# Kernel tuning notes

Hardware: AMD Instinct MI355X
Metric: run time of the kernel (lower is better)

## Reference

```python
import jax, jax.numpy as jnp
import numpy as np

B, S, D = 4, 2048, 1024
H = 16
KD = 1024  # key_dim (total)
VD = 1024  # value_dim (total)


def setup_inputs() -> dict:
    key = jax.random.key(0)
    ks = jax.random.split(key, 8)
    queries = jax.random.normal(ks[0], (B, S, D), dtype=jnp.float32)
    keys_ = jax.random.normal(ks[1], (B, S, D), dtype=jnp.float32)
    values = jax.random.normal(ks[2], (B, S, D), dtype=jnp.float32)
    # causal float mask (1 = keep, 0 = masked), broadcasts over [B, H, S, S]
    mask = jnp.tril(jnp.ones((S, S), dtype=jnp.float32))[None, None]
    # Linear weights stored as [in, out] so forward is x @ W
    Wq = jax.random.normal(ks[3], (D, KD), dtype=jnp.float32) / np.sqrt(D)
    Wk = jax.random.normal(ks[4], (D, KD), dtype=jnp.float32) / np.sqrt(D)
    Wv = jax.random.normal(ks[5], (D, VD), dtype=jnp.float32) / np.sqrt(D)
    Wo = jax.random.normal(ks[6], (H * VD // H * H // H * 1 if False else VD, D), dtype=jnp.float32) / np.sqrt(VD)
    bo = jnp.zeros((D,), dtype=jnp.float32)
    return {"queries": queries, "keys": keys_, "values": values, "mask": mask,
            "Wq": Wq, "Wk": Wk, "Wv": Wv, "Wo": Wo, "bo": bo}


def reference(queries, keys, values, mask, Wq, Wk, Wv, Wo, bo):
    b, s, _ = queries.shape
    # project then split heads: [B, S, H, hd] -> [B, H, S, hd]
    q = (queries @ Wq).reshape(b, s, H, -1).transpose(0, 2, 1, 3)
    k = (keys @ Wk).reshape(b, s, H, -1).transpose(0, 2, 1, 3)
    v = (values @ Wv).reshape(b, s, H, -1).transpose(0, 2, 1, 3)
    dk = k.shape[-1]  # per-head key dim (scale uses post-split dk, as in source)
    logits = jnp.einsum('bhqd,bhkd->bhqk', q, k) / jnp.sqrt(jnp.float32(dk))
    logits = logits + (1.0 - mask) * (-1e9)
    attn = jax.nn.softmax(logits, axis=-1)  # dropout p=0 in eval -> identity
    o = jnp.einsum('bhqk,bhkd->bhqd', attn, v)
    o = o.transpose(0, 2, 1, 3).reshape(b, s, H * (VD // H))
    return o @ Wo + bo
```

## Files before the change

kernel.cpp:

```cpp
#include <hip/hip_runtime.h>
#include <hip/hip_bf16.h>

typedef __attribute__((ext_vector_type(8))) short s8v;
typedef __attribute__((ext_vector_type(4))) short s4v;
typedef __attribute__((ext_vector_type(4))) float f4v;

#define S_LEN 2048
#define NH 16
#define HD 64
#define DMODEL 1024
#define KVB 64
#define LOG2E 1.44269504088896f
#define FIXMAX 32.0f

__device__ __forceinline__ unsigned short f2bf(float f) {
  union { float f; unsigned int u; } v; v.f = f;
  return (unsigned short)((v.u + 0x7FFFu + ((v.u >> 16) & 1u)) >> 16);
}

__device__ __forceinline__ f4v mfma16(s8v a, s8v b, f4v c) {
  return __builtin_amdgcn_mfma_f32_16x16x32_bf16(a, b, c, 0, 0, 0);
}

__device__ __forceinline__ void gl_lds16(const unsigned short* g, unsigned short* l) {
  __builtin_amdgcn_global_load_lds(
      (const __attribute__((address_space(1))) void*)g,
      (__attribute__((address_space(3))) void*)l, 16, 0, 0);
}

__global__ __launch_bounds__(256)
void cast3(const float* __restrict__ a, const float* __restrict__ b,
           const float* __restrict__ c, unsigned short* __restrict__ oa,
           unsigned short* __restrict__ ob, unsigned short* __restrict__ oc,
           int n8) {
  const float* src = (blockIdx.y == 0) ? a : (blockIdx.y == 1) ? b : c;
  unsigned short* dst = (blockIdx.y == 0) ? oa : (blockIdx.y == 1) ? ob : oc;
  for (int i = blockIdx.x * 256 + threadIdx.x; i < n8; i += gridDim.x * 256) {
    f4v v0 = *(const f4v*)(src + (size_t)i * 8);
    f4v v1 = *(const f4v*)(src + (size_t)i * 8 + 4);
    unsigned short cv[8];
#pragma unroll
    for (int j = 0; j < 4; j++) { cv[j] = f2bf(v0[j]); cv[4 + j] = f2bf(v1[j]); }
    *(s8v*)(dst + (size_t)i * 8) = *(const s8v*)cv;
  }
}

__global__ __launch_bounds__(256)
void transpose_cast4(const float* __restrict__ w0, const float* __restrict__ w1,
                     const float* __restrict__ w2, const float* __restrict__ w3,
                     unsigned short* __restrict__ o0, unsigned short* __restrict__ o1,
                     unsigned short* __restrict__ o2, unsigned short* __restrict__ o3) {
  __shared__ float tile[32][33];
  const int z = blockIdx.z;
  const float* W = (z == 0) ? w0 : (z == 1) ? w1 : (z == 2) ? w2 : w3;
  unsigned short* Wt = (z == 0) ? o0 : (z == 1) ? o1 : (z == 2) ? o2 : o3;
  int x = threadIdx.x, y = threadIdx.y;
  int n0 = blockIdx.x * 32, k0 = blockIdx.y * 32;
#pragma unroll
  for (int i = 0; i < 32; i += 8)
    tile[y + i][x] = W[(size_t)(k0 + y + i) * DMODEL + n0 + x];
  __syncthreads();
#pragma unroll
  for (int i = 0; i < 32; i += 8)
    Wt[(size_t)(n0 + y + i) * DMODEL + k0 + x] = f2bf(tile[x][y + i]);
}

__global__ __launch_bounds__(256, 2)
void qkv_gemm(const unsigned short* __restrict__ Qc, const unsigned short* __restrict__ Kc,
              const unsigned short* __restrict__ Vc, const unsigned short* __restrict__ WqT,
              const unsigned short* __restrict__ WkT, const unsigned short* __restrict__ WvT,
              unsigned short* __restrict__ Qb, unsigned short* __restrict__ Kb,
              unsigned short* __restrict__ Vtb) {
  __shared__ unsigned short As[128 * 32];
  __shared__ unsigned short Bs[128 * 32];
  const int z = blockIdx.z;
  const unsigned short* A = (z == 0) ? Qc : (z == 1) ? Kc : Vc;
  const unsigned short* Bt = (z == 0) ? WqT : (z == 1) ? WkT : WvT;
  unsigned short* C = (z == 0) ? Qb : (z == 1) ? Kb : Vtb;
  const float scale = (z == 0) ? 0.125f * LOG2E : 1.0f;

  const int t = threadIdx.x;
  const int l = t & 63;
  const int w = t >> 6, wr = w >> 1, wc = w & 1;
  const int m0 = blockIdx.x * 128, n0 = blockIdx.y * 128;
  const int lg = l >> 4, lm = l & 15;

  f4v acc[4][4];
#pragma unroll
  for (int i = 0; i < 4; i++)
#pragma unroll
    for (int j = 0; j < 4; j++) acc[i][j] = f4v{0.f, 0.f, 0.f, 0.f};

  const int srow = t >> 2;
  const int scol = (t & 3) * 8;
  const unsigned short* Arow = A + (size_t)(m0 + srow) * DMODEL + scol;
  const unsigned short* Brow = Bt + (size_t)(n0 + srow) * DMODEL + scol;
  unsigned short* AsW = &As[w * 512];
  unsigned short* BsW = &Bs[w * 512];

  for (int k0 = 0; k0 < DMODEL; k0 += 32) {
    gl_lds16(Arow + k0, AsW);
    gl_lds16(Arow + (size_t)64 * DMODEL + k0, AsW + 2048);
    gl_lds16(Brow + k0, BsW);
    gl_lds16(Brow + (size_t)64 * DMODEL + k0, BsW + 2048);
    __syncthreads();

    s8v af[4], bf[4];
#pragma unroll
    for (int mi = 0; mi < 4; mi++)
      af[mi] = *(const s8v*)&As[(wr * 64 + mi * 16 + lm) * 32 + lg * 8];
#pragma unroll
    for (int ni = 0; ni < 4; ni++)
      bf[ni] = *(const s8v*)&Bs[(wc * 64 + ni * 16 + lm) * 32 + lg * 8];
#pragma unroll
    for (int mi = 0; mi < 4; mi++)
#pragma unroll
      for (int ni = 0; ni < 4; ni++)
        acc[mi][ni] = mfma16(af[mi], bf[ni], acc[mi][ni]);
    __syncthreads();
  }

#pragma unroll
  for (int mi = 0; mi < 4; mi++)
#pragma unroll
    for (int ni = 0; ni < 4; ni++) {
      int col = n0 + wc * 64 + ni * 16 + lm;
#pragma unroll
      for (int rr = 0; rr < 4; rr++) {
        int row = m0 + wr * 64 + mi * 16 + lg * 4 + rr;
        unsigned short h = f2bf(acc[mi][ni][rr] * scale);
        int b = row >> 11, s = row & 2047, hh = col >> 6, d = col & 63;
        if (z < 2)
          C[(((size_t)(b * NH + hh)) * S_LEN + s) * HD + d] = h;
        else
          C[(((size_t)(b * NH + hh)) * HD + d) * S_LEN + s] = h;
      }
    }
}

__global__ __launch_bounds__(256, 2)
void out_gemm(const unsigned short* __restrict__ A, const unsigned short* __restrict__ Bt,
              float* __restrict__ Cp, const float* __restrict__ bias) {
  __shared__ unsigned short As[128 * 32];
  __shared__ unsigned short Bs[128 * 32];
  const int t = threadIdx.x;
  const int l = t & 63;
  const int w = t >> 6, wr = w >> 1, wc = w & 1;
  const int m0 = blockIdx.x * 128, n0 = blockIdx.y * 128;
  const int lg = l >> 4, lm = l & 15;

  f4v acc[4][4];
#pragma unroll
  for (int i = 0; i < 4; i++)
#pragma unroll
    for (int j = 0; j < 4; j++) acc[i][j] = f4v{0.f, 0.f, 0.f, 0.f};

  const int srow = t >> 2;
  const int scol = (t & 3) * 8;
  const unsigned short* Arow = A + (size_t)(m0 + srow) * DMODEL + scol;
  const unsigned short* Brow = Bt + (size_t)(n0 + srow) * DMODEL + scol;
  unsigned short* AsW = &As[w * 512];
  unsigned short* BsW = &Bs[w * 512];

  for (int k0 = 0; k0 < DMODEL; k0 += 32) {
    gl_lds16(Arow + k0, AsW);
    gl_lds16(Arow + (size_t)64 * DMODEL + k0, AsW + 2048);
    gl_lds16(Brow + k0, BsW);
    gl_lds16(Brow + (size_t)64 * DMODEL + k0, BsW + 2048);
    __syncthreads();

    s8v af[4], bf[4];
#pragma unroll
    for (int mi = 0; mi < 4; mi++)
      af[mi] = *(const s8v*)&As[(wr * 64 + mi * 16 + lm) * 32 + lg * 8];
#pragma unroll
    for (int ni = 0; ni < 4; ni++)
      bf[ni] = *(const s8v*)&Bs[(wc * 64 + ni * 16 + lm) * 32 + lg * 8];
#pragma unroll
    for (int mi = 0; mi < 4; mi++)
#pragma unroll
      for (int ni = 0; ni < 4; ni++)
        acc[mi][ni] = mfma16(af[mi], bf[ni], acc[mi][ni]);
    __syncthreads();
  }

#pragma unroll
  for (int mi = 0; mi < 4; mi++)
#pragma unroll
    for (int ni = 0; ni < 4; ni++) {
      int col = n0 + wc * 64 + ni * 16 + lm;
      float bv = bias[col];
#pragma unroll
      for (int rr = 0; rr < 4; rr++) {
        int row = m0 + wr * 64 + mi * 16 + lg * 4 + rr;
        Cp[(size_t)row * DMODEL + col] = acc[mi][ni][rr] + bv;
      }
    }
}

__global__ __launch_bounds__(256, 2)
void attn_k(const unsigned short* __restrict__ Q, const unsigned short* __restrict__ Km,
            const unsigned short* __restrict__ Vt, unsigned short* __restrict__ O) {
  __shared__ unsigned short Ks[2][KVB * HD];
  __shared__ unsigned short Vs[2][HD * KVB];
  __shared__ unsigned short pbuf[16][16 * KVB];
  const int t = threadIdx.x, l = t & 63, w = t >> 6;
  const int lg = l >> 4, lm = l & 15;

  const int c = blockIdx.x;
  const int bh = c & 63;
  const int pr4 = (c >> 6) & 3;
  const int pr = (c >> 8) ? 7 - pr4 : pr4;
  const int s0A = (15 - pr) * 128, s0B = pr * 128;

  const unsigned short* Qh = Q + (size_t)bh * S_LEN * HD;
  const unsigned short* Kh = Km + (size_t)bh * S_LEN * HD;
  const unsigned short* Vh = Vt + (size_t)bh * HD * S_LEN;

  const int xo0 = (lg ^ (lm & 7)) << 4;
  const int xo1 = ((4 + lg) ^ (lm & 7)) << 4;

  const int q00 = s0A + w * 32, q01 = q00 + 16;
  const int q02 = s0B + w * 32, q03 = q02 + 16;

  s8v qf0[2], qf1[2], qf2[2], qf3[2];
#define LOADQ(QF, Q0)                                                   \
  QF[0] = *(const s8v*)(Qh + (size_t)((Q0) + lm) * HD + lg * 8);        \
  QF[1] = *(const s8v*)(Qh + (size_t)((Q0) + lm) * HD + 32 + lg * 8);
  LOADQ(qf0, q00) LOADQ(qf1, q01) LOADQ(qf2, q02) LOADQ(qf3, q03)
#undef LOADQ

  f4v o0[4], o1[4], o2[4], o3[4];
#pragma unroll
  for (int i = 0; i < 4; i++) {
    o0[i] = f4v{0.f, 0.f, 0.f, 0.f}; o1[i] = f4v{0.f, 0.f, 0.f, 0.f};
    o2[i] = f4v{0.f, 0.f, 0.f, 0.f}; o3[i] = f4v{0.f, 0.f, 0.f, 0.f};
  }
  float l0_ = 0.f, l1_ = 0.f, l2_ = 0.f, l3_ = 0.f;

  const int sr0 = w * 8 + (l >> 3);
  const int sj = l & 7;

#define STAGE(buf, kv)                                                          \
  {                                                                             \
    _Pragma("unroll")                                                           \
    for (int i = 0; i < 2; i++) {                                               \
      int r_ = sr0 + i * 32;                                                    \
      int jj_ = ((sj ^ (r_ & 7)) << 3);                                         \
      gl_lds16(Kh + (size_t)((kv) + r_) * HD + jj_, &Ks[buf][w * 512 + i * 2048]); \
      gl_lds16(Vh + (size_t)r_ * S_LEN + (kv) + jj_, &Vs[buf][w * 512 + i * 2048]); \
    }                                                                           \
  }

#define TILE_S(QF, LL, Q0, PI)                                                  \
  {                                                                             \
    const int dt = (Q0) >> 6;                                                   \
    if (ti <= dt) {                                                             \
      f4v s_[4];                                                                \
      _Pragma("unroll")                                                         \
      for (int sub = 0; sub < 4; sub++) {                                       \
        s_[sub] = f4v{0.f, 0.f, 0.f, 0.f};                                      \
        s_[sub] = mfma16(kf[sub * 2], QF[0], s_[sub]);                          \
        s_[sub] = mfma16(kf[sub * 2 + 1], QF[1], s_[sub]);                      \
      }                                                                         \
      if (ti == dt) {                                                           \
        const int qrow = (Q0) + lm;                                             \
        _Pragma("unroll")                                                       \
        for (int sub = 0; sub < 4; sub++) {                                     \
          const int kbase = kv + sub * 16 + lg * 4;                             \
          _Pragma("unroll")                                                     \
          for (int rr = 0; rr < 4; rr++)                                        \
            if (kbase + rr > qrow) s_[sub][rr] = -1e30f;                        \
        }                                                                       \
      }                                                                         \
      char* pb_ = (char*)pbuf[w * 4 + PI];                                      \
      float psum = 0.f;                                                         \
      _Pragma("unroll")                                                         \
      for (int sub = 0; sub < 4; sub++) {                                       \
        float p0 = exp2f(s_[sub][0] - FIXMAX);                                  \
        float p1 = exp2f(s_[sub][1] - FIXMAX);                                  \
        float p2 = exp2f(s_[sub][2] - FIXMAX);                                  \
        float p3 = exp2f(s_[sub][3] - FIXMAX);                                  \
        psum += (p0 + p1) + (p2 + p3);                                          \
        unsigned int u01, u23;                                                  \
        asm("v_cvt_pk_bf16_f32 %0, %1, %2" : "=v"(u01) : "v"(p0), "v"(p1));     \
        asm("v_cvt_pk_bf16_f32 %0, %1, %2" : "=v"(u23) : "v"(p2), "v"(p3));     \
        const int cc = (sub * 4 + lg) ^ ((lm & 7) << 1);                        \
        uint2 pv; pv.x = u01; pv.y = u23;                                       \
        *(uint2*)(pb_ + lm * 128 + (cc << 3)) = pv;                             \
      }                                                                         \
      (LL) += psum;                                                             \
    }                                                                           \
  }

#define TILE_PV(OO, Q0, PI)                                                     \
  {                                                                             \
    const int dt = (Q0) >> 6;                                                   \
    if (ti <= dt) {                                                             \
      const char* pb_ = (const char*)pbuf[w * 4 + PI];                          \
      s8v pf0 = *(const s8v*)(pb_ + lm * 128 + xo0);                            \
      s8v pf1 = *(const s8v*)(pb_ + lm * 128 + xo1);                            \
      _Pragma("unroll")                                                         \
      for (int nc = 0; nc < 4; nc++) {                                          \
        OO[nc] = mfma16(vf[nc * 2], pf0, OO[nc]);                               \
        OO[nc] = mfma16(vf[nc * 2 + 1], pf1, OO[nc]);                           \
      }                                                                         \
    }                                                                           \
  }

  const int nt = 2 * (15 - pr) + 2;
  int cur = 0;
  STAGE(0, 0);
  __syncthreads();

  for (int ti = 0; ti < nt; ++ti) {
    const int kv = ti * 64;
    if (ti + 1 < nt) STAGE(cur ^ 1, kv + 64);

    const unsigned short* Kb = Ks[cur];
    const unsigned short* Vb = Vs[cur];

    s8v kf[8];
#pragma unroll
    for (int sub = 0; sub < 4; sub++) {
      const char* krow = (const char*)Kb + (sub * 16 + lm) * 128;
      kf[sub * 2] = *(const s8v*)(krow + xo0);
      kf[sub * 2 + 1] = *(const s8v*)(krow + xo1);
    }

    TILE_S(qf0, l0_, q00, 0);
    TILE_S(qf1, l1_, q01, 1);
    TILE_S(qf2, l2_, q02, 2);
    TILE_S(qf3, l3_, q03, 3);

    __builtin_amdgcn_sched_barrier(0);

    s8v vf[8];
#pragma unroll
    for (int sub = 0; sub < 4; sub++) {
      const char* vrow = (const char*)Vb + (sub * 16 + lm) * 128;
      vf[sub * 2] = *(const s8v*)(vrow + xo0);
      vf[sub * 2 + 1] = *(const s8v*)(vrow + xo1);
    }

    TILE_PV(o0, q00, 0);
    TILE_PV(o1, q01, 1);
    TILE_PV(o2, q02, 2);
    TILE_PV(o3, q03, 3);

    __syncthreads();
    cur ^= 1;
  }

  const int b = bh >> 4, hh = bh & 15;
#define EPI(OO, LL, Q0)                                                         \
  {                                                                             \
    float lt = (LL);                                                            \
    lt += __shfl_xor(lt, 16);                                                   \
    lt += __shfl_xor(lt, 32);                                                   \
    const float inv = 1.f / lt;                                                 \
    unsigned short* Orow =                                                      \
        O + ((size_t)b * S_LEN + (Q0) + lm) * DMODEL + hh * HD;                 \
    _Pragma("unroll")                                                           \
    for (int nc = 0; nc < 4; nc++) {                                            \
      unsigned short h4[4];                                                     \
      _Pragma("unroll")                                                         \
      for (int rr = 0; rr < 4; rr++) h4[rr] = f2bf(OO[nc][rr] * inv);           \
      *(s4v*)(Orow + nc * 16 + lg * 4) = *(const s4v*)h4;                       \
    }                                                                           \
  }
  EPI(o0, l0_, q00);
  EPI(o1, l1_, q01);
  EPI(o2, l2_, q02);
  EPI(o3, l3_, q03);
#undef EPI
#undef TILE_PV
#undef TILE_S
#undef STAGE
}

extern "C" void kernel_launch(void* const* d_in, const int* in_sizes, int n_in,
                              void* d_out, int out_size, void* d_ws, size_t ws_size,
                              hipStream_t stream) {
  const float* queries = (const float*)d_in[0];
  const float* keys = (const float*)d_in[1];
  const float* values = (const float*)d_in[2];
  const float* Wq = (const float*)d_in[4];
  const float* Wk = (const float*)d_in[5];
  const float* Wv = (const float*)d_in[6];
  const float* Wo = (const float*)d_in[7];
  const float* bo = (const float*)d_in[8];

  char* ws = (char*)d_ws;
  const size_t WB = (size_t)DMODEL * DMODEL * 2;
  unsigned short* WqT = (unsigned short*)(ws + 0 * WB);
  unsigned short* WkT = (unsigned short*)(ws + 1 * WB);
  unsigned short* WvT = (unsigned short*)(ws + 2 * WB);
  unsigned short* WoT = (unsigned short*)(ws + 3 * WB);
  const size_t TB = (size_t)4 * S_LEN * DMODEL * 2;
  unsigned short* Qb  = (unsigned short*)(ws + 4 * WB);
  unsigned short* Kb  = (unsigned short*)(ws + 4 * WB + TB);
  unsigned short* Vtb = (unsigned short*)(ws + 4 * WB + 2 * TB);
  unsigned short* Ob  = (unsigned short*)(ws + 4 * WB + 3 * TB);
  unsigned short* Qc  = (unsigned short*)(ws + 4 * WB + 4 * TB);
  unsigned short* Kc  = (unsigned short*)(ws + 4 * WB + 5 * TB);
  unsigned short* Vc  = (unsigned short*)(ws + 4 * WB + 6 * TB);

  const int M = 4 * S_LEN;

  cast3<<<dim3(2048, 3), 256, 0, stream>>>(queries, keys, values, Qc, Kc, Vc,
                                           M * DMODEL / 8);

  transpose_cast4<<<dim3(32, 32, 4), dim3(32, 8), 0, stream>>>(
      Wq, Wk, Wv, Wo, WqT, WkT, WvT, WoT);

  qkv_gemm<<<dim3(64, 8, 3), 256, 0, stream>>>(Qc, Kc, Vc, WqT, WkT, WvT,
                                               Qb, Kb, Vtb);

  attn_k<<<512, 256, 0, stream>>>(Qb, Kb, Vtb, Ob);

  out_gemm<<<dim3(64, 8), 256, 0, stream>>>(Ob, WoT, (float*)d_out, bo);
}
```

Baseline: 210.0 us.

## Widen GEMM K-tile to 64 with XOR-swizzled LDS layout in shared body

```diff
diff --git a/kernel.cpp b/kernel.cpp
--- a/kernel.cpp
+++ b/kernel.cpp
@@ -65,137 +65,114 @@
     Wt[(size_t)(n0 + y + i) * DMODEL + k0 + x] = f2bf(tile[x][y + i]);
 }
 
+template <typename Epi>
+__device__ __forceinline__ void gemm_body(const unsigned short* __restrict__ A_,
+                                          const unsigned short* __restrict__ Bt_,
+                                          Epi epi) {
+  __shared__ unsigned short As[128 * 64];
+  __shared__ unsigned short Bs[128 * 64];
+  const int t = threadIdx.x;
+  const int l = t & 63;
+  const int w = t >> 6, wr = w >> 1, wc = w & 1;
+  const int m0 = blockIdx.x * 128, n0 = blockIdx.y * 128;
+  const int lg = l >> 4, lm = l & 15;
+
+  f4v acc[4][4];
+#pragma unroll
+  for (int i = 0; i < 4; i++)
+#pragma unroll
+    for (int j = 0; j < 4; j++) acc[i][j] = f4v{0.f, 0.f, 0.f, 0.f};
+
+  const int sgc = (l & 7) ^ ((l >> 3) & 7);
+  const unsigned short* Aprow = A_ + (size_t)(m0 + w * 8 + (l >> 3)) * DMODEL + sgc * 8;
+  const unsigned short* Bprow = Bt_ + (size_t)(n0 + w * 8 + (l >> 3)) * DMODEL + sgc * 8;
+  const int xo0 = (lg ^ (lm & 7)) << 4;
+  const int xo1 = ((4 + lg) ^ (lm & 7)) << 4;
+
+  for (int k0 = 0; k0 < DMODEL; k0 += 64) {
+#pragma unroll
+    for (int i = 0; i < 4; i++) {
+      gl_lds16(Aprow + (size_t)(i * 32) * DMODEL + k0, &As[i * 2048 + w * 512]);
+      gl_lds16(Bprow + (size_t)(i * 32) * DMODEL + k0, &Bs[i * 2048 + w * 512]);
+    }
+    __syncthreads();
+
+    s8v af[4][2], bf[4][2];
+#pragma unroll
+    for (int mi = 0; mi < 4; mi++) {
+      const char* ar = (const char*)As + (wr * 64 + mi * 16 + lm) * 128;
+      af[mi][0] = *(const s8v*)(ar + xo0);
+      af[mi][1] = *(const s8v*)(ar + xo1);
+    }
+#pragma unroll
+    for (int ni = 0; ni < 4; ni++) {
+      const char* br = (const char*)Bs + (wc * 64 + ni * 16 + lm) * 128;
+      bf[ni][0] = *(const s8v*)(br + xo0);
+      bf[ni][1] = *(const s8v*)(br + xo1);
+    }
+#pragma unroll
+    for (int mi = 0; mi < 4; mi++)
+#pragma unroll
+      for (int ni = 0; ni < 4; ni++) {
+        acc[mi][ni] = mfma16(af[mi][0], bf[ni][0], acc[mi][ni]);
+        acc[mi][ni] = mfma16(af[mi][1], bf[ni][1], acc[mi][ni]);
+      }
+    __syncthreads();
+  }
+  epi(acc, m0, n0, wr, wc, lg, lm);
+}
+
 __global__ __launch_bounds__(256, 2)
 void qkv_gemm(const unsigned short* __restrict__ Qc, const unsigned short* __restrict__ Kc,
               const unsigned short* __restrict__ Vc, const unsigned short* __restrict__ WqT,
               const unsigned short* __restrict__ WkT, const unsigned short* __restrict__ WvT,
               unsigned short* __restrict__ Qb, unsigned short* __restrict__ Kb,
               unsigned short* __restrict__ Vtb) {
-  __shared__ unsigned short As[128 * 32];
-  __shared__ unsigned short Bs[128 * 32];
   const int z = blockIdx.z;
   const unsigned short* A = (z == 0) ? Qc : (z == 1) ? Kc : Vc;
   const unsigned short* Bt = (z == 0) ? WqT : (z == 1) ? WkT : WvT;
   unsigned short* C = (z == 0) ? Qb : (z == 1) ? Kb : Vtb;
   const float scale = (z == 0) ? 0.125f * LOG2E : 1.0f;
 
-  const int t = threadIdx.x;
-  const int l = t & 63;
-  const int w = t >> 6, wr = w >> 1, wc = w & 1;
-  const int m0 = blockIdx.x * 128, n0 = blockIdx.y * 128;
-  const int lg = l >> 4, lm = l & 15;
-
-  f4v acc[4][4];
-#pragma unroll
-  for (int i = 0; i < 4; i++)
-#pragma unroll
-    for (int j = 0; j < 4; j++) acc[i][j] = f4v{0.f, 0.f, 0.f, 0.f};
-
-  const int srow = t >> 2;
-  const int scol = (t & 3) * 8;
-  const unsigned short* Arow = A + (size_t)(m0 + srow) * DMODEL + scol;
-  const unsigned short* Brow = Bt + (size_t)(n0 + srow) * DMODEL + scol;
-  unsigned short* AsW = &As[w * 512];
-  unsigned short* BsW = &Bs[w * 512];
-
-  for (int k0 = 0; k0 < DMODEL; k0 += 32) {
-    gl_lds16(Arow + k0, AsW);
-    gl_lds16(Arow + (size_t)64 * DMODEL + k0, AsW + 2048);
-    gl_lds16(Brow + k0, BsW);
-    gl_lds16(Brow + (size_t)64 * DMODEL + k0, BsW + 2048);
-    __syncthreads();
-
-    s8v af[4], bf[4];
+  gemm_body(A, Bt, [&](f4v (&acc)[4][4], int m0, int n0, int wr, int wc,
+                       int lg, int lm) {
 #pragma unroll
     for (int mi = 0; mi < 4; mi++)
-      af[mi] = *(const s8v*)&As[(wr * 64 + mi * 16 + lm) * 32 + lg * 8];
-#pragma unroll
-    for (int ni = 0; ni < 4; ni++)
-      bf[ni] = *(const s8v*)&Bs[(wc * 64 + ni * 16 + lm) * 32 + lg * 8];
-#pragma unroll
-    for (int mi = 0; mi < 4; mi++)
-#pragma unroll
-      for (int ni = 0; ni < 4; ni++)
-        acc[mi][ni] = mfma16(af[mi], bf[ni], acc[mi][ni]);
-    __syncthreads();
-  }
-
-#pragma unroll
-  for (int mi = 0; mi < 4; mi++)
-#pragma unroll
-    for (int ni = 0; ni < 4; ni++) {
-      int col = n0 + wc * 64 + ni * 16 + lm;
-#pragma unroll
-      for (int rr = 0; rr < 4; rr++) {
-        int row = m0 + wr * 64 + mi * 16 + lg * 4 + rr;
-        unsigned short h = f2bf(acc[mi][ni][rr] * scale);
-        int b = row >> 11, s = row & 2047, hh = col >> 6, d = col & 63;
-        if (z < 2)
-          C[(((size_t)(b * NH + hh)) * S_LEN + s) * HD + d] = h;
-        else
-          C[(((size_t)(b * NH + hh)) * HD + d) * S_LEN + s] = h;
+#pragma unroll
+      for (int ni = 0; ni < 4; ni++) {
+        int col = n0 + wc * 64 + ni * 16 + lm;
+#pragma unroll
+        for (int rr = 0; rr < 4; rr++) {
+          int row = m0 + wr * 64 + mi * 16 + lg * 4 + rr;
+          unsigned short h = f2bf(acc[mi][ni][rr] * scale);
+          int b = row >> 11, s = row & 2047, hh = col >> 6, d = col & 63;
+          if (z < 2)
+            C[(((size_t)(b * NH + hh)) * S_LEN + s) * HD + d] = h;
+          else
+            C[(((size_t)(b * NH + hh)) * HD + d) * S_LEN + s] = h;
+        }
       }
-    }
+  });
 }
 
 __global__ __launch_bounds__(256, 2)
 void out_gemm(const unsigned short* __restrict__ A, const unsigned short* __restrict__ Bt,
               float* __restrict__ Cp, const float* __restrict__ bias) {
-  __shared__ unsigned short As[128 * 32];
-  __shared__ unsigned short Bs[128 * 32];
-  const int t = threadIdx.x;
-  const int l = t & 63;
-  const int w = t >> 6, wr = w >> 1, wc = w & 1;
-  const int m0 = blockIdx.x * 128, n0 = blockIdx.y * 128;
-  const int lg = l >> 4, lm = l & 15;
-
-  f4v acc[4][4];
-#pragma unroll
-  for (int i = 0; i < 4; i++)
-#pragma unroll
-    for (int j = 0; j < 4; j++) acc[i][j] = f4v{0.f, 0.f, 0.f, 0.f};
-
-  const int srow = t >> 2;
-  const int scol = (t & 3) * 8;
-  const unsigned short* Arow = A + (size_t)(m0 + srow) * DMODEL + scol;
-  const unsigned short* Brow = Bt + (size_t)(n0 + srow) * DMODEL + scol;
-  unsigned short* AsW = &As[w * 512];
-  unsigned short* BsW = &Bs[w * 512];
-
-  for (int k0 = 0; k0 < DMODEL; k0 += 32) {
-    gl_lds16(Arow + k0, AsW);
-    gl_lds16(Arow + (size_t)64 * DMODEL + k0, AsW + 2048);
-    gl_lds16(Brow + k0, BsW);
-    gl_lds16(Brow + (size_t)64 * DMODEL + k0, BsW + 2048);
-    __syncthreads();
-
-    s8v af[4], bf[4];
+  gemm_body(A, Bt, [&](f4v (&acc)[4][4], int m0, int n0, int wr, int wc,
+                       int lg, int lm) {
 #pragma unroll
     for (int mi = 0; mi < 4; mi++)
-      af[mi] = *(const s8v*)&As[(wr * 64 + mi * 16 + lm) * 32 + lg * 8];
-#pragma unroll
-    for (int ni = 0; ni < 4; ni++)
-      bf[ni] = *(const s8v*)&Bs[(wc * 64 + ni * 16 + lm) * 32 + lg * 8];
-#pragma unroll
-    for (int mi = 0; mi < 4; mi++)
-#pragma unroll
-      for (int ni = 0; ni < 4; ni++)
-        acc[mi][ni] = mfma16(af[mi], bf[ni], acc[mi][ni]);
-    __syncthreads();
-  }
-
-#pragma unroll
-  for (int mi = 0; mi < 4; mi++)
-#pragma unroll
-    for (int ni = 0; ni < 4; ni++) {
-      int col = n0 + wc * 64 + ni * 16 + lm;
-      float bv = bias[col];
-#pragma unroll
-      for (int rr = 0; rr < 4; rr++) {
-        int row = m0 + wr * 64 + mi * 16 + lg * 4 + rr;
-        Cp[(size_t)row * DMODEL + col] = acc[mi][ni][rr] + bv;
+#pragma unroll
+      for (int ni = 0; ni < 4; ni++) {
+        int col = n0 + wc * 64 + ni * 16 + lm;
+        float bv = bias[col];
+#pragma unroll
+        for (int rr = 0; rr < 4; rr++) {
+          int row = m0 + wr * 64 + mi * 16 + lg * 4 + rr;
+          Cp[(size_t)row * DMODEL + col] = acc[mi][ni][rr] + bv;
+        }
       }
-    }
+  });
 }
 
 __global__ __launch_bounds__(256, 2)
```

New measurement: 185.4 us. -11.7%, faster.
